# Kernel tuning notes

Measured on AMD Instinct MI355X. Metric: run time of the kernel, lower is better.

## Reference

```python
import jax, jax.numpy as jnp
import numpy as np

L, B, T, D, H, HS, VS, HID = 4, 4, 1024, 1024, 16, 64, 64, 4096
EPS = 1e-6
MASK_NEG = -2.3819763e38


def rms_norm(x, scale):
    # flax nn.RMSNorm: x * rsqrt(mean(x^2) + eps) * scale
    return x * jax.lax.rsqrt(jnp.mean(jnp.square(x), axis=-1, keepdims=True) + EPS) * scale


def apply_rope(x, max_wavelength=10000):
    # x: [B, T, H, hd]
    *_, seq_len, num_heads, head_dim = x.shape
    fraction = 2 * jnp.arange(0, head_dim // 2) / head_dim
    timescale = max_wavelength ** fraction
    positions = jnp.arange(seq_len, dtype=x.dtype)
    sinusoid_inp = positions[:, None] / timescale[None, :]
    sinusoid_inp = sinusoid_inp[..., None, :]  # [T, 1, hd/2]
    sin = jnp.sin(sinusoid_inp)
    cos = jnp.cos(sinusoid_inp)
    first_half, second_half = jnp.split(x, 2, axis=-1)
    first_part = first_half * cos - second_half * sin
    second_part = second_half * cos + first_half * sin
    return jnp.concatenate([first_part, second_part], axis=-1).astype(x.dtype)


def setup_inputs() -> dict:
    key = jax.random.key(0)
    ks = jax.random.split(key, 16)
    s = 0.02

    def n(k, shape):
        return jax.random.normal(k, shape, jnp.float32) * s

    return {
        "x": jax.random.normal(ks[0], (B, T, D), jnp.float32),
        "mask": jnp.ones((B, T), dtype=bool),
        "Wq": n(ks[1], (L, D, H * HS)), "bq": n(ks[2], (L, H * HS)),
        "Wk": n(ks[3], (L, D, H * HS)), "bk": n(ks[4], (L, H * HS)),
        "Wv": n(ks[5], (L, D, H * VS)), "bv": n(ks[6], (L, H * VS)),
        "Wo": n(ks[7], (L, H * VS, D)), "bo": n(ks[8], (L, D)),
        "q_scale": jnp.ones((L, HS), jnp.float32),
        "k_scale": jnp.ones((L, HS), jnp.float32),
        "ln1_scale": jnp.ones((L, D), jnp.float32),
        "ln2_scale": jnp.ones((L, D), jnp.float32),
        "Wg": n(ks[9], (L, D, HID)),
        "W1": n(ks[10], (L, D, HID)),
        "W2": n(ks[11], (L, HID, D)),
    }


def reference(x, mask, Wq, bq, Wk, bk, Wv, bv, Wo, bo, q_scale, k_scale,
              ln1_scale, ln2_scale, Wg, W1, W2):
    # self-attention mask: [B, 1, T, T]
    self_mask = mask[:, None, :, None] & mask[:, None, None, :]
    # positionwise mask: [B, T, 1]
    pos_mask = self_mask.any(axis=-1, keepdims=True)[:, 0]
    inv_sqrt = np.float32(1.0 / np.sqrt(HS))

    for l in range(L):
        # pre-attention RMSNorm
        x_ln = rms_norm(x, ln1_scale[l])
        # Q/K/V projections -> [B, T, H, hd], with per-head RMSNorm + RoPE on Q,K
        q = (x_ln @ Wq[l] + bq[l]).reshape(B, T, H, HS)
        q = apply_rope(rms_norm(q, q_scale[l]))
        k = (x_ln @ Wk[l] + bk[l]).reshape(B, T, H, HS)
        k = apply_rope(rms_norm(k, k_scale[l]))
        v = (x_ln @ Wv[l] + bv[l]).reshape(B, T, H, VS)
        # attention logits [B, H, T, T]
        logits = jnp.einsum('bthd,bThd->bhtT', q, k) * inv_sqrt
        logits = jnp.where(self_mask, logits, MASK_NEG)
        w = jax.nn.softmax(logits)
        w = jnp.where(self_mask, w, 0)
        attn = jnp.einsum('bhtT,bThd->bthd', w, v).reshape(B, T, H * VS)
        x = x + attn @ Wo[l] + bo[l]
        # gated FFN (GELU gate)
        x2 = rms_norm(x, ln2_scale[l])
        gate = jax.nn.gelu(x2 @ Wg[l])
        x = x + (gate * (x2 @ W1[l])) @ W2[l]
        x = jnp.where(pos_mask, x, 0)
    return x
```

## Files before the change

kernel.cpp:

```cpp
#include <hip/hip_runtime.h>

#define DI __device__ __forceinline__

typedef __attribute__((ext_vector_type(8))) __bf16 bf16x8;
typedef __attribute__((ext_vector_type(4))) float f32x4;
typedef __attribute__((ext_vector_type(4))) unsigned int u32x4;
typedef __attribute__((ext_vector_type(4))) unsigned short u16x4;

static constexpr int Bc = 4, Tc = 1024, Dc = 1024, Hc = 16, HSc = 64, HIDc = 4096, Lc = 4;

DI unsigned short f2bf(float f) {
    union { float f; unsigned int u; } c; c.f = f;
    unsigned int u = c.u;
    u += 0x7fffu + ((u >> 16) & 1u);
    return (unsigned short)(u >> 16);
}
DI float bf2f(unsigned short h) {
    union { unsigned int u; float f; } c; c.u = ((unsigned int)h) << 16;
    return c.f;
}

DI void gload_lds16(const void* g, void* l) {
    __builtin_amdgcn_global_load_lds((const __attribute__((address_space(1))) void*)g,
                                     (__attribute__((address_space(3))) void*)l, 16, 0, 0);
}

DI f32x4 mfma16x16x32(bf16x8 a, bf16x8 b, f32x4 c) {
    return __builtin_amdgcn_mfma_f32_16x16x32_bf16(a, b, c, 0, 0, 0);
}

__global__ __launch_bounds__(256) void transpose_cast_kernel(const float* __restrict__ W,
                                                             unsigned short* __restrict__ Wt,
                                                             int K, int N, size_t lstride, int rowOff) {
    __shared__ float tile[32][33];
    const int l = blockIdx.z;
    const float* Wl = W + (size_t)l * K * N;
    unsigned short* Wtl = Wt + (size_t)l * lstride;
    const int n0 = blockIdx.x * 32, k0 = blockIdx.y * 32;
    const int tx = threadIdx.x, ty = threadIdx.y;
#pragma unroll
    for (int i = 0; i < 32; i += 8) tile[ty + i][tx] = Wl[(size_t)(k0 + ty + i) * N + (n0 + tx)];
    __syncthreads();
#pragma unroll
    for (int i = 0; i < 32; i += 8)
        Wtl[(size_t)(rowOff + n0 + ty + i) * K + (k0 + tx)] = f2bf(tile[tx][ty + i]);
}

__global__ __launch_bounds__(256) void copy_f32_kernel(const float* __restrict__ in,
                                                       float* __restrict__ out, int n4) {
    const int i = blockIdx.x * 256 + threadIdx.x;
    if (i < n4) ((f32x4*)out)[i] = ((const f32x4*)in)[i];
}

__global__ __launch_bounds__(256) void reduce_res_kernel(const float* __restrict__ p0,
                                                         const float* __restrict__ p1,
                                                         float* __restrict__ xres, int n4) {
    const int i = blockIdx.x * 256 + threadIdx.x;
    if (i < n4) {
        const f32x4 a = ((const f32x4*)p0)[i];
        const f32x4 b = ((const f32x4*)p1)[i];
        f32x4 r = ((f32x4*)xres)[i];
        r[0] += a[0] + b[0]; r[1] += a[1] + b[1]; r[2] += a[2] + b[2]; r[3] += a[3] + b[3];
        ((f32x4*)xres)[i] = r;
    }
}

__global__ __launch_bounds__(256) void rope_table_kernel(float* __restrict__ cosT,
                                                         float* __restrict__ sinT) {
    const int idx = blockIdx.x * 256 + threadIdx.x;
    const int t = idx >> 5, j = idx & 31;
    const float ts = powf(10000.f, (float)(2 * j) * (1.f / 64.f));
    const float ang = (float)t / ts;
    sinT[idx] = sinf(ang);
    cosT[idx] = cosf(ang);
}

__global__ __launch_bounds__(256) void rmsnorm_kernel(const float* __restrict__ x,
                                                      const float* __restrict__ scale,
                                                      unsigned short* __restrict__ out) {
    const int row = blockIdx.x;
    const int tid = threadIdx.x;
    const f32x4 v = ((const f32x4*)(x + (size_t)row * Dc))[tid];
    float ss = v[0] * v[0] + v[1] * v[1] + v[2] * v[2] + v[3] * v[3];
#pragma unroll
    for (int m = 32; m; m >>= 1) ss += __shfl_xor(ss, m);
    __shared__ float red[4];
    if ((tid & 63) == 0) red[tid >> 6] = ss;
    __syncthreads();
    const float tot = red[0] + red[1] + red[2] + red[3];
    const float r = rsqrtf(tot * (1.f / (float)Dc) + 1e-6f);
    const f32x4 sc = ((const f32x4*)scale)[tid];
    u16x4 o;
    o[0] = f2bf(v[0] * r * sc[0]);
    o[1] = f2bf(v[1] * r * sc[1]);
    o[2] = f2bf(v[2] * r * sc[2]);
    o[3] = f2bf(v[3] * r * sc[3]);
    *((u16x4*)(out + (size_t)row * Dc) + tid) = o;
}

__global__ __launch_bounds__(256) void rmsnorm_add_kernel(float* __restrict__ xres,
                                                          const float* __restrict__ p0,
                                                          const float* __restrict__ p1,
                                                          const float* __restrict__ scale,
                                                          unsigned short* __restrict__ out) {
    const int row = blockIdx.x;
    const int tid = threadIdx.x;
    const size_t base = (size_t)row * Dc;
    f32x4 v = ((const f32x4*)(xres + base))[tid];
    const f32x4 a = ((const f32x4*)(p0 + base))[tid];
    const f32x4 b = ((const f32x4*)(p1 + base))[tid];
    v[0] += a[0] + b[0]; v[1] += a[1] + b[1]; v[2] += a[2] + b[2]; v[3] += a[3] + b[3];
    ((f32x4*)(xres + base))[tid] = v;
    float ss = v[0] * v[0] + v[1] * v[1] + v[2] * v[2] + v[3] * v[3];
#pragma unroll
    for (int m = 32; m; m >>= 1) ss += __shfl_xor(ss, m);
    __shared__ float red[4];
    if ((tid & 63) == 0) red[tid >> 6] = ss;
    __syncthreads();
    const float tot = red[0] + red[1] + red[2] + red[3];
    const float r = rsqrtf(tot * (1.f / (float)Dc) + 1e-6f);
    const f32x4 sc = ((const f32x4*)scale)[tid];
    u16x4 o;
    o[0] = f2bf(v[0] * r * sc[0]);
    o[1] = f2bf(v[1] * r * sc[1]);
    o[2] = f2bf(v[2] * r * sc[2]);
    o[3] = f2bf(v[3] * r * sc[3]);
    *((u16x4*)(out + (size_t)row * Dc) + tid) = o;
}

__global__ __launch_bounds__(256) void qk_rope_kernel(unsigned short* __restrict__ q,
                                                      unsigned short* __restrict__ k,
                                                      const float* __restrict__ qscale,
                                                      const float* __restrict__ kscale,
                                                      const float* __restrict__ cosT,
                                                      const float* __restrict__ sinT) {
    unsigned short* buf = blockIdx.y ? k : q;
    const float* scl = blockIdx.y ? kscale : qscale;
    const int tid = threadIdx.x;
    const int sub = tid & 7;
    const size_t row = (size_t)blockIdx.x * 32 + (tid >> 3);
    const int t = (int)((row >> 4) & (size_t)(Tc - 1));
    unsigned short* qr = buf + row * 64;
    const u32x4 pk = *(const u32x4*)(qr + sub * 8);
    float v[8];
#pragma unroll
    for (int i = 0; i < 4; ++i) {
        v[2 * i] = bf2f((unsigned short)(pk[i] & 0xffffu));
        v[2 * i + 1] = bf2f((unsigned short)(pk[i] >> 16));
    }
    float ss = 0.f;
#pragma unroll
    for (int i = 0; i < 8; ++i) ss += v[i] * v[i];
    ss += __shfl_xor(ss, 1, 8);
    ss += __shfl_xor(ss, 2, 8);
    ss += __shfl_xor(ss, 4, 8);
    const float rn = rsqrtf(ss * (1.f / 64.f) + 1e-6f);
    const f32x4 sc0 = ((const f32x4*)scl)[sub * 2];
    const f32x4 sc1 = ((const f32x4*)scl)[sub * 2 + 1];
    float xn[8];
#pragma unroll
    for (int i = 0; i < 8; ++i) xn[i] = v[i] * rn * (i < 4 ? sc0[i] : sc1[i - 4]);
    float other[8];
#pragma unroll
    for (int i = 0; i < 8; ++i) other[i] = __shfl_xor(xn[i], 4, 8);
    const int jb = (sub & 3) * 8;
    const f32x4 c0 = *(const f32x4*)(cosT + t * 32 + jb);
    const f32x4 c1 = *(const f32x4*)(cosT + t * 32 + jb + 4);
    const f32x4 s0 = *(const f32x4*)(sinT + t * 32 + jb);
    const f32x4 s1 = *(const f32x4*)(sinT + t * 32 + jb + 4);
    u32x4 o;
#pragma unroll
    for (int i = 0; i < 4; ++i) {
        const float ca = (2 * i < 4) ? c0[2 * i] : c1[2 * i - 4];
        const float cb = (2 * i + 1 < 4) ? c0[2 * i + 1] : c1[2 * i - 3];
        const float sa = (2 * i < 4) ? s0[2 * i] : s1[2 * i - 4];
        const float sb = (2 * i + 1 < 4) ? s0[2 * i + 1] : s1[2 * i - 3];
        float oa, ob;
        if (sub < 4) { oa = xn[2 * i] * ca - other[2 * i] * sa; ob = xn[2 * i + 1] * cb - other[2 * i + 1] * sb; }
        else         { oa = xn[2 * i] * ca + other[2 * i] * sa; ob = xn[2 * i + 1] * cb + other[2 * i + 1] * sb; }
        o[i] = (unsigned int)f2bf(oa) | ((unsigned int)f2bf(ob) << 16);
    }
    *(u32x4*)(qr + sub * 8) = o;
}

__global__ __launch_bounds__(256) void vtrans_kernel(const unsigned short* __restrict__ v,
                                                     unsigned short* __restrict__ vt) {
    __shared__ unsigned short tile[32][33];
    const int bh = blockIdx.z, b = bh >> 4, h = bh & 15;
    const int t0 = blockIdx.x * 32, d0 = blockIdx.y * 32;
    const int tx = threadIdx.x, ty = threadIdx.y;
#pragma unroll
    for (int i = 0; i < 32; i += 8)
        tile[ty + i][tx] = v[(((size_t)b * Tc + (t0 + ty + i)) * Hc + h) * 64 + (d0 + tx)];
    __syncthreads();
#pragma unroll
    for (int i = 0; i < 32; i += 8)
        vt[(((size_t)b * Hc + h) * 64 + (d0 + ty + i)) * Tc + (t0 + tx)] = tile[tx][ty + i];
}

template <int EPI>
__global__ __launch_bounds__(256, 3) void gemm_bt_kernel(
    const unsigned short* __restrict__ A, const unsigned short* __restrict__ Bt,
    const float* __restrict__ bias0, const float* __restrict__ bias1, const float* __restrict__ bias2,
    unsigned short* __restrict__ out0, unsigned short* __restrict__ out1, unsigned short* __restrict__ out2,
    const float* __restrict__ resin, float* __restrict__ resout,
    int N, int K, int KZ, size_t zstride, int nbn) {
    __shared__ unsigned short As[128 * 64];
    __shared__ unsigned short Bs[128 * 64];
    const int tid = threadIdx.x, w = tid >> 6, l = tid & 63;
    const int wr = w >> 1, wc = w & 1;
    const int nwg = gridDim.x;
    const int t = (blockIdx.x & 7) * (nwg >> 3) + (blockIdx.x >> 3);
    const int st = t >> 6, r = t & 63;
    const int nsn = nbn >> 3;
    const int sm = st / nsn, sn = st - sm * nsn;
    const int bm = sm * 8 + (r >> 3), bn = sn * 8 + (r & 7);
    const int kz = blockIdx.z;

    const unsigned short* Ag = A + (size_t)bm * 128 * K + (size_t)kz * KZ;
    const unsigned short* Bg = Bt + (size_t)bn * 128 * K + (size_t)kz * KZ;
    const int nk = KZ >> 6;
    const int srow = (l >> 3);
    const int slc = (l & 7);

    f32x4 acc[4][4] = {};
    for (int kt = 0; kt < nk; ++kt) {
#pragma unroll
        for (int p = 0; p < 4; ++p) {
            const int row = w * 8 + p * 32 + srow;
            const int ce = slc ^ (row & 7);
            gload_lds16(Ag + (size_t)row * K + kt * 64 + ce * 8, &As[(w * 8 + p * 32) * 64]);
            gload_lds16(Bg + (size_t)row * K + kt * 64 + ce * 8, &Bs[(w * 8 + p * 32) * 64]);
        }
        __syncthreads();
        bf16x8 av[4][2], bv[4][2];
#pragma unroll
        for (int mf = 0; mf < 4; ++mf)
#pragma unroll
            for (int ks = 0; ks < 2; ++ks) {
                const int arow = wr * 64 + mf * 16 + (l & 15);
                av[mf][ks] = *(const bf16x8*)&As[arow * 64 + (((ks * 4 + (l >> 4)) ^ (arow & 7)) << 3)];
                const int brow = wc * 64 + mf * 16 + (l & 15);
                bv[mf][ks] = *(const bf16x8*)&Bs[brow * 64 + (((ks * 4 + (l >> 4)) ^ (brow & 7)) << 3)];
            }
#pragma unroll
        for (int mf = 0; mf < 4; ++mf)
#pragma unroll
            for (int nf = 0; nf < 4; ++nf)
#pragma unroll
                for (int ks = 0; ks < 2; ++ks)
                    acc[mf][nf] = mfma16x16x32(av[mf][ks], bv[nf][ks], acc[mf][nf]);
        __syncthreads();
    }

    const int r0 = bm * 128 + wr * 64 + ((l >> 4) << 2);
    if constexpr (EPI == 0) {
        const int sel = bn >> 3;
        const float* bias = sel == 0 ? bias0 : (sel == 1 ? bias1 : bias2);
        unsigned short* o = sel == 0 ? out0 : (sel == 1 ? out1 : out2);
        const int cb = (bn & 7) * 128 + wc * 64 + (l & 15);
#pragma unroll
        for (int nf = 0; nf < 4; ++nf) {
            const int col = cb + nf * 16;
            const float bvv = bias[col];
#pragma unroll
            for (int mf = 0; mf < 4; ++mf)
#pragma unroll
                for (int g = 0; g < 4; ++g)
                    o[(size_t)(r0 + mf * 16 + g) * 1024 + col] = f2bf(acc[mf][nf][g] + bvv);
        }
    } else {
        const int c0 = bn * 128 + wc * 64 + (l & 15);
        const size_t zoff = (size_t)kz * zstride;
#pragma unroll
        for (int nf = 0; nf < 4; ++nf) {
            const int col = c0 + nf * 16;
            float bvv = 0.f;
            if constexpr (EPI == 1) {
                if (bias0) bvv = bias0[col];
            }
#pragma unroll
            for (int mf = 0; mf < 4; ++mf)
#pragma unroll
                for (int g = 0; g < 4; ++g) {
                    const size_t idx = (size_t)(r0 + mf * 16 + g) * N + col;
                    const float val = acc[mf][nf][g];
                    if constexpr (EPI == 1) {
                        resout[idx] = resin[idx] + val + bvv;
                    } else {
                        resout[zoff + idx] = val;
                    }
                }
        }
    }
}

__global__ __launch_bounds__(512, 4) void gemm_mlp_kernel(
    const unsigned short* __restrict__ A, const unsigned short* __restrict__ Bg_,
    const unsigned short* __restrict__ Bu_, unsigned short* __restrict__ out,
    int N, int K, int nbn) {
    __shared__ unsigned short lds[3 * 128 * 64];
    unsigned short* As = lds;
    unsigned short* Gs = lds + 128 * 64;
    unsigned short* Us = lds + 2 * 128 * 64;
    const int tid = threadIdx.x, w = tid >> 6, l = tid & 63;
    const int isUp = w >> 2;
    const int wq = w & 3;
    const int wr = wq >> 1, wc = wq & 1;
    const int nwg = gridDim.x;
    const int t = (blockIdx.x & 7) * (nwg >> 3) + (blockIdx.x >> 3);
    const int st = t >> 6, r = t & 63;
    const int nsn = nbn >> 3;
    const int sm = st / nsn, sn = st - sm * nsn;
    const int bm = sm * 8 + (r >> 3), bn = sn * 8 + (r & 7);

    const unsigned short* AgK = A + (size_t)bm * 128 * K;
    const unsigned short* GgK = Bg_ + (size_t)bn * 128 * K;
    const unsigned short* UgK = Bu_ + (size_t)bn * 128 * K;
    const unsigned short* Bs_my = isUp ? Us : Gs;
    const int nk = K >> 6;
    const int lr = l >> 3, slc = l & 7;

    f32x4 acc[4][4] = {};
    for (int kt = 0; kt < nk; ++kt) {
#pragma unroll
        for (int p = 0; p < 2; ++p) {
            const int rbase = p * 64 + w * 8;
            const int row = rbase + lr;
            const int ce = slc ^ (row & 7);
            gload_lds16(AgK + (size_t)row * K + kt * 64 + ce * 8, As + rbase * 64);
            gload_lds16(GgK + (size_t)row * K + kt * 64 + ce * 8, Gs + rbase * 64);
            gload_lds16(UgK + (size_t)row * K + kt * 64 + ce * 8, Us + rbase * 64);
        }
        __syncthreads();
#pragma unroll
        for (int ks = 0; ks < 2; ++ks) {
            bf16x8 av[4], bv[4];
#pragma unroll
            for (int mf = 0; mf < 4; ++mf) {
                const int arow = wr * 64 + mf * 16 + (l & 15);
                av[mf] = *(const bf16x8*)&As[arow * 64 + (((ks * 4 + (l >> 4)) ^ (arow & 7)) << 3)];
                const int brow = wc * 64 + mf * 16 + (l & 15);
                bv[mf] = *(const bf16x8*)&Bs_my[brow * 64 + (((ks * 4 + (l >> 4)) ^ (brow & 7)) << 3)];
            }
#pragma unroll
            for (int mf = 0; mf < 4; ++mf)
#pragma unroll
                for (int nf = 0; nf < 4; ++nf)
                    acc[mf][nf] = mfma16x16x32(av[mf], bv[nf], acc[mf][nf]);
        }
        __syncthreads();
    }

    unsigned short* P = lds;
    const int rl0 = wr * 64 + ((l >> 4) << 2);
    const int cl0 = wc * 64 + (l & 15);
    if (!isUp) {
#pragma unroll
        for (int nf = 0; nf < 4; ++nf)
#pragma unroll
            for (int mf = 0; mf < 4; ++mf)
#pragma unroll
                for (int g = 0; g < 4; ++g) {
                    const float gvl = acc[mf][nf][g];
                    const float z = 0.7978845608028654f * (gvl + 0.044715f * gvl * gvl * gvl);
                    P[(rl0 + mf * 16 + g) * 132 + cl0 + nf * 16] = f2bf(0.5f * gvl * (1.f + tanhf(z)));
                }
    }
    __syncthreads();
    if (isUp) {
        const int r0 = bm * 128 + rl0;
        const int c0 = bn * 128 + cl0;
#pragma unroll
        for (int nf = 0; nf < 4; ++nf)
#pragma unroll
            for (int mf = 0; mf < 4; ++mf)
#pragma unroll
                for (int g = 0; g < 4; ++g) {
                    const float p = bf2f(P[(rl0 + mf * 16 + g) * 132 + cl0 + nf * 16]);
                    out[(size_t)(r0 + mf * 16 + g) * N + (c0 + nf * 16)] = f2bf(p * acc[mf][nf][g]);
                }
    }
}

__global__ __launch_bounds__(256, 2) void attn_kernel(const unsigned short* __restrict__ q,
                                                      const unsigned short* __restrict__ k,
                                                      const unsigned short* __restrict__ vt,
                                                      unsigned short* __restrict__ o) {
    constexpr int ST = 72;
    __shared__ unsigned short Qs[64 * ST], Ks[64 * ST], Vs[64 * ST], Ps[64 * ST];
    const int qb = blockIdx.x, h = blockIdx.y, b = blockIdx.z;
    const int tid = threadIdx.x, wid = tid >> 6, lane = tid & 63;
    const size_t qkbase = ((size_t)b << 20) + ((size_t)h << 6);
    const size_t vbase = ((size_t)(b * 16 + h)) << 16;
#pragma unroll
    for (int p = 0; p < 2; ++p) {
        const int cid = tid + p * 256, r = cid >> 3, c = cid & 7;
        *(u32x4*)&Qs[r * ST + c * 8] =
            *(const u32x4*)&q[qkbase + (size_t)(qb * 64 + r) * 1024 + c * 8];
    }
    f32x4 oacc[4] = {};
    float mrun[4], lrun[4];
#pragma unroll
    for (int g = 0; g < 4; ++g) { mrun[g] = -1e30f; lrun[g] = 0.f; }
    const int fr = lane & 15, ko = (lane >> 4) * 8;
    u32x4 kr[2], vr[2];
#pragma unroll
    for (int p = 0; p < 2; ++p) {
        const int cid = tid + p * 256, r = cid >> 3, c = cid & 7;
        kr[p] = *(const u32x4*)&k[qkbase + (size_t)(r) * 1024 + c * 8];
        vr[p] = *(const u32x4*)&vt[vbase + (size_t)r * 1024 + c * 8];
    }
    for (int j = 0; j < 16; ++j) {
        __syncthreads();
#pragma unroll
        for (int p = 0; p < 2; ++p) {
            const int cid = tid + p * 256, r = cid >> 3, c = cid & 7;
            *(u32x4*)&Ks[r * ST + c * 8] = kr[p];
            *(u32x4*)&Vs[r * ST + c * 8] = vr[p];
        }
        __syncthreads();
        if (j < 15) {
#pragma unroll
            for (int p = 0; p < 2; ++p) {
                const int cid = tid + p * 256, r = cid >> 3, c = cid & 7;
                kr[p] = *(const u32x4*)&k[qkbase + (size_t)((j + 1) * 64 + r) * 1024 + c * 8];
                vr[p] = *(const u32x4*)&vt[vbase + (size_t)r * 1024 + (j + 1) * 64 + c * 8];
            }
        }
        f32x4 sacc[4] = {};
#pragma unroll
        for (int ks = 0; ks < 2; ++ks) {
            const bf16x8 a = *(const bf16x8*)&Qs[(wid * 16 + fr) * ST + ks * 32 + ko];
#pragma unroll
            for (int n = 0; n < 4; ++n) {
                const bf16x8 bb = *(const bf16x8*)&Ks[(n * 16 + fr) * ST + ks * 32 + ko];
                sacc[n] = mfma16x16x32(a, bb, sacc[n]);
            }
        }
        float s[4][4];
#pragma unroll
        for (int n = 0; n < 4; ++n)
#pragma unroll
            for (int g = 0; g < 4; ++g) s[n][g] = sacc[n][g] * 0.125f;
        float rmax[4];
#pragma unroll
        for (int g = 0; g < 4; ++g)
            rmax[g] = fmaxf(fmaxf(s[0][g], s[1][g]), fmaxf(s[2][g], s[3][g]));
#pragma unroll
        for (int msk = 1; msk < 16; msk <<= 1)
#pragma unroll
            for (int g = 0; g < 4; ++g) rmax[g] = fmaxf(rmax[g], __shfl_xor(rmax[g], msk));
        float mn[4], alpha[4], rsum[4];
#pragma unroll
        for (int g = 0; g < 4; ++g) {
            mn[g] = fmaxf(mrun[g], rmax[g]);
            alpha[g] = __expf(mrun[g] - mn[g]);
            mrun[g] = mn[g];
            rsum[g] = 0.f;
        }
#pragma unroll
        for (int n = 0; n < 4; ++n)
#pragma unroll
            for (int g = 0; g < 4; ++g) {
                const float p = __expf(s[n][g] - mn[g]);
                rsum[g] += p;
                Ps[(wid * 16 + (lane >> 4) * 4 + g) * ST + n * 16 + (lane & 15)] = f2bf(p);
            }
#pragma unroll
        for (int msk = 1; msk < 16; msk <<= 1)
#pragma unroll
            for (int g = 0; g < 4; ++g) rsum[g] += __shfl_xor(rsum[g], msk);
#pragma unroll
        for (int g = 0; g < 4; ++g) lrun[g] = lrun[g] * alpha[g] + rsum[g];
#pragma unroll
        for (int nd = 0; nd < 4; ++nd)
#pragma unroll
            for (int g = 0; g < 4; ++g) oacc[nd][g] *= alpha[g];
#pragma unroll
        for (int ks = 0; ks < 2; ++ks) {
            const bf16x8 a = *(const bf16x8*)&Ps[(wid * 16 + fr) * ST + ks * 32 + ko];
#pragma unroll
            for (int nd = 0; nd < 4; ++nd) {
                const bf16x8 bb = *(const bf16x8*)&Vs[(nd * 16 + fr) * ST + ks * 32 + ko];
                oacc[nd] = mfma16x16x32(a, bb, oacc[nd]);
            }
        }
    }
#pragma unroll
    for (int nd = 0; nd < 4; ++nd)
#pragma unroll
        for (int g = 0; g < 4; ++g) {
            const int r = qb * 64 + wid * 16 + (lane >> 4) * 4 + g;
            o[qkbase + (size_t)r * 1024 + nd * 16 + (lane & 15)] = f2bf(oacc[nd][g] / lrun[g]);
        }
}

extern "C" void kernel_launch(void* const* d_in, const int* in_sizes, int n_in,
                              void* d_out, int out_size, void* d_ws, size_t ws_size,
                              hipStream_t stream) {
    (void)in_sizes; (void)n_in; (void)out_size; (void)ws_size;
    const float* x   = (const float*)d_in[0];
    const float* Wq  = (const float*)d_in[2];
    const float* bq  = (const float*)d_in[3];
    const float* Wk  = (const float*)d_in[4];
    const float* bk  = (const float*)d_in[5];
    const float* Wv  = (const float*)d_in[6];
    const float* bv  = (const float*)d_in[7];
    const float* Wo  = (const float*)d_in[8];
    const float* bo  = (const float*)d_in[9];
    const float* qsc = (const float*)d_in[10];
    const float* ksc = (const float*)d_in[11];
    const float* ln1 = (const float*)d_in[12];
    const float* ln2 = (const float*)d_in[13];
    const float* Wg  = (const float*)d_in[14];
    const float* W1  = (const float*)d_in[15];
    const float* W2  = (const float*)d_in[16];
    float* xres = (float*)d_out;

    char* wsb = (char*)d_ws;
    size_t off = 0;
    auto alloc = [&](size_t bytes) -> char* {
        char* p = wsb + off;
        off += (bytes + 255) & ~(size_t)255;
        return p;
    };
    const size_t WQKV = (size_t)Lc * 3 * Dc * Dc;
    const size_t WPROJ = (size_t)Lc * Dc * Hc * HSc;
    const size_t WMLP  = (size_t)Lc * Dc * HIDc;
    unsigned short* wqkvT = (unsigned short*)alloc(WQKV * 2);
    unsigned short* woT = (unsigned short*)alloc(WPROJ * 2);
    unsigned short* wgT = (unsigned short*)alloc(WMLP * 2);
    unsigned short* w1T = (unsigned short*)alloc(WMLP * 2);
    unsigned short* w2T = (unsigned short*)alloc(WMLP * 2);
    float* ropeC = (float*)alloc((size_t)Tc * 32 * 4);
    float* ropeS = (float*)alloc((size_t)Tc * 32 * 4);
    unsigned short* xln  = (unsigned short*)alloc((size_t)Bc * Tc * Dc * 2);
    unsigned short* qbuf = (unsigned short*)alloc((size_t)Bc * Tc * Hc * HSc * 2);
    unsigned short* kbuf = (unsigned short*)alloc((size_t)Bc * Tc * Hc * HSc * 2);
    unsigned short* vbuf = (unsigned short*)alloc((size_t)Bc * Tc * Hc * HSc * 2);
    unsigned short* vtg  = (unsigned short*)alloc((size_t)Bc * Hc * HSc * Tc * 2);
    unsigned short* hbuf = (unsigned short*)alloc((size_t)Bc * Tc * HIDc * 2);
    float* psum = (float*)alloc((size_t)2 * Bc * Tc * Dc * 4);

    const dim3 b32(32, 8);
    const size_t qkvStride = (size_t)3 * Dc * Dc;
    transpose_cast_kernel<<<dim3(32, 32, 4), b32, 0, stream>>>(Wq, wqkvT, 1024, 1024, qkvStride, 0);
    transpose_cast_kernel<<<dim3(32, 32, 4), b32, 0, stream>>>(Wk, wqkvT, 1024, 1024, qkvStride, 1024);
    transpose_cast_kernel<<<dim3(32, 32, 4), b32, 0, stream>>>(Wv, wqkvT, 1024, 1024, qkvStride, 2048);
    transpose_cast_kernel<<<dim3(32, 32, 4), b32, 0, stream>>>(Wo, woT, 1024, 1024, (size_t)Dc * Dc, 0);
    transpose_cast_kernel<<<dim3(128, 32, 4), b32, 0, stream>>>(Wg, wgT, 1024, 4096, (size_t)Dc * HIDc, 0);
    transpose_cast_kernel<<<dim3(128, 32, 4), b32, 0, stream>>>(W1, w1T, 1024, 4096, (size_t)Dc * HIDc, 0);
    transpose_cast_kernel<<<dim3(32, 128, 4), b32, 0, stream>>>(W2, w2T, 4096, 1024, (size_t)Dc * HIDc, 0);
    rope_table_kernel<<<128, 256, 0, stream>>>(ropeC, ropeS);
    copy_f32_kernel<<<4096, 256, 0, stream>>>(x, xres, (Bc * Tc * Dc) / 4);

    const size_t zstr = (size_t)Bc * Tc * Dc;
    for (int l = 0; l < Lc; ++l) {
        const unsigned short* wqkv_l = wqkvT + (size_t)l * qkvStride;
        const unsigned short* wo_l = woT + (size_t)l * Dc * Dc;
        const unsigned short* wg_l = wgT + (size_t)l * Dc * HIDc;
        const unsigned short* w1_l = w1T + (size_t)l * Dc * HIDc;
        const unsigned short* w2_l = w2T + (size_t)l * Dc * HIDc;

        if (l == 0)
            rmsnorm_kernel<<<4096, 256, 0, stream>>>(xres, ln1 + l * Dc, xln);
        else
            rmsnorm_add_kernel<<<4096, 256, 0, stream>>>(xres, psum, psum + zstr, ln1 + l * Dc, xln);
        gemm_bt_kernel<0><<<768, 256, 0, stream>>>(
            xln, wqkv_l, bq + l * 1024, bk + l * 1024, bv + l * 1024,
            qbuf, kbuf, vbuf, nullptr, nullptr, 3072, 1024, 1024, 0, 24);
        qk_rope_kernel<<<dim3(2048, 2), 256, 0, stream>>>(qbuf, kbuf, qsc + l * 64, ksc + l * 64,
                                                          ropeC, ropeS);
        vtrans_kernel<<<dim3(32, 2, 64), b32, 0, stream>>>(vbuf, vtg);
        attn_kernel<<<dim3(16, 16, 4), 256, 0, stream>>>(qbuf, kbuf, vtg, xln);
        gemm_bt_kernel<1><<<256, 256, 0, stream>>>(
            xln, wo_l, bo + l * 1024, nullptr, nullptr,
            nullptr, nullptr, nullptr, xres, xres, 1024, 1024, 1024, 0, 8);
        rmsnorm_kernel<<<4096, 256, 0, stream>>>(xres, ln2 + l * Dc, xln);
        gemm_mlp_kernel<<<1024, 512, 0, stream>>>(xln, wg_l, w1_l, hbuf, 4096, 1024, 32);
        gemm_bt_kernel<4><<<dim3(256, 1, 2), 256, 0, stream>>>(
            hbuf, w2_l, nullptr, nullptr, nullptr,
            nullptr, nullptr, nullptr, nullptr, psum, 1024, 4096, 2048, zstr, 8);
    }
    reduce_res_kernel<<<4096, 256, 0, stream>>>(psum, psum + zstr, xres, (int)(zstr / 4));
}
```

Baseline: 1.221 ms.

## Enlarge attention query tile to 128 rows with 512 threads and MFMA priority

Measured after the change: 1.203 ms. About the same (-1.5%).

```diff
diff --git a/kernel.cpp b/kernel.cpp
--- a/kernel.cpp
+++ b/kernel.cpp
@@ -383,52 +383,42 @@
     }
 }
 
-__global__ __launch_bounds__(256, 2) void attn_kernel(const unsigned short* __restrict__ q,
+__global__ __launch_bounds__(512, 4) void attn_kernel(const unsigned short* __restrict__ q,
                                                       const unsigned short* __restrict__ k,
                                                       const unsigned short* __restrict__ vt,
                                                       unsigned short* __restrict__ o) {
     constexpr int ST = 72;
-    __shared__ unsigned short Qs[64 * ST], Ks[64 * ST], Vs[64 * ST], Ps[64 * ST];
+    __shared__ unsigned short Qs[128 * ST], Ks[64 * ST], Vs[64 * ST], Ps[128 * ST];
     const int qb = blockIdx.x, h = blockIdx.y, b = blockIdx.z;
     const int tid = threadIdx.x, wid = tid >> 6, lane = tid & 63;
     const size_t qkbase = ((size_t)b << 20) + ((size_t)h << 6);
     const size_t vbase = ((size_t)(b * 16 + h)) << 16;
 #pragma unroll
     for (int p = 0; p < 2; ++p) {
-        const int cid = tid + p * 256, r = cid >> 3, c = cid & 7;
+        const int cid = tid + p * 512, r = cid >> 3, c = cid & 7;
         *(u32x4*)&Qs[r * ST + c * 8] =
-            *(const u32x4*)&q[qkbase + (size_t)(qb * 64 + r) * 1024 + c * 8];
+            *(const u32x4*)&q[qkbase + (size_t)(qb * 128 + r) * 1024 + c * 8];
     }
     f32x4 oacc[4] = {};
     float mrun[4], lrun[4];
 #pragma unroll
     for (int g = 0; g < 4; ++g) { mrun[g] = -1e30f; lrun[g] = 0.f; }
     const int fr = lane & 15, ko = (lane >> 4) * 8;
-    u32x4 kr[2], vr[2];
-#pragma unroll
-    for (int p = 0; p < 2; ++p) {
-        const int cid = tid + p * 256, r = cid >> 3, c = cid & 7;
-        kr[p] = *(const u32x4*)&k[qkbase + (size_t)(r) * 1024 + c * 8];
-        vr[p] = *(const u32x4*)&vt[vbase + (size_t)r * 1024 + c * 8];
-    }
+    const int sr = tid >> 3, sc = tid & 7;
+    u32x4 kr, vr;
+    kr = *(const u32x4*)&k[qkbase + (size_t)sr * 1024 + sc * 8];
+    vr = *(const u32x4*)&vt[vbase + (size_t)sr * 1024 + sc * 8];
     for (int j = 0; j < 16; ++j) {
         __syncthreads();
-#pragma unroll
-        for (int p = 0; p < 2; ++p) {
-            const int cid = tid + p * 256, r = cid >> 3, c = cid & 7;
-            *(u32x4*)&Ks[r * ST + c * 8] = kr[p];
-            *(u32x4*)&Vs[r * ST + c * 8] = vr[p];
-        }
+        *(u32x4*)&Ks[sr * ST + sc * 8] = kr;
+        *(u32x4*)&Vs[sr * ST + sc * 8] = vr;
         __syncthreads();
         if (j < 15) {
-#pragma unroll
-            for (int p = 0; p < 2; ++p) {
-                const int cid = tid + p * 256, r = cid >> 3, c = cid & 7;
-                kr[p] = *(const u32x4*)&k[qkbase + (size_t)((j + 1) * 64 + r) * 1024 + c * 8];
-                vr[p] = *(const u32x4*)&vt[vbase + (size_t)r * 1024 + (j + 1) * 64 + c * 8];
-            }
+            kr = *(const u32x4*)&k[qkbase + (size_t)((j + 1) * 64 + sr) * 1024 + sc * 8];
+            vr = *(const u32x4*)&vt[vbase + (size_t)sr * 1024 + (j + 1) * 64 + sc * 8];
         }
         f32x4 sacc[4] = {};
+        __builtin_amdgcn_s_setprio(1);
 #pragma unroll
         for (int ks = 0; ks < 2; ++ks) {
             const bf16x8 a = *(const bf16x8*)&Qs[(wid * 16 + fr) * ST + ks * 32 + ko];
@@ -438,6 +428,7 @@
                 sacc[n] = mfma16x16x32(a, bb, sacc[n]);
             }
         }
+        __builtin_amdgcn_s_setprio(0);
         float s[4][4];
 #pragma unroll
         for (int n = 0; n < 4; ++n)
@@ -477,6 +468,7 @@
         for (int nd = 0; nd < 4; ++nd)
 #pragma unroll
             for (int g = 0; g < 4; ++g) oacc[nd][g] *= alpha[g];
+        __builtin_amdgcn_s_setprio(1);
 #pragma unroll
         for (int ks = 0; ks < 2; ++ks) {
             const bf16x8 a = *(const bf16x8*)&Ps[(wid * 16 + fr) * ST + ks * 32 + ko];
@@ -486,12 +478,13 @@
                 oacc[nd] = mfma16x16x32(a, bb, oacc[nd]);
             }
         }
+        __builtin_amdgcn_s_setprio(0);
     }
 #pragma unroll
     for (int nd = 0; nd < 4; ++nd)
 #pragma unroll
         for (int g = 0; g < 4; ++g) {
-            const int r = qb * 64 + wid * 16 + (lane >> 4) * 4 + g;
+            const int r = qb * 128 + wid * 16 + (lane >> 4) * 4 + g;
             o[qkbase + (size_t)r * 1024 + nd * 16 + (lane & 15)] = f2bf(oacc[nd][g] / lrun[g]);
         }
 }
@@ -573,7 +566,7 @@
         qk_rope_kernel<<<dim3(2048, 2), 256, 0, stream>>>(qbuf, kbuf, qsc + l * 64, ksc + l * 64,
                                                           ropeC, ropeS);
         vtrans_kernel<<<dim3(32, 2, 64), b32, 0, stream>>>(vbuf, vtg);
-        attn_kernel<<<dim3(16, 16, 4), 256, 0, stream>>>(qbuf, kbuf, vtg, xln);
+        attn_kernel<<<dim3(8, 16, 4), 512, 0, stream>>>(qbuf, kbuf, vtg, xln);
         gemm_bt_kernel<1><<<256, 256, 0, stream>>>(
             xln, wo_l, bo + l * 1024, nullptr, nullptr,
             nullptr, nullptr, nullptr, xres, xres, 1024, 1024, 1024, 0, 8);
```
